# Performance work log

Hardware: AMD Instinct MI355X
Metric: run time of the kernel (lower is better)

## Reference

```python
import jax, jax.numpy as jnp
import numpy as np

B, T, C = 8, 1024, 768
NH = 12
HD = C // NH  # 64


def setup_inputs() -> dict:
    key = jax.random.key(0)
    k1, k2, k3 = jax.random.split(key, 3)
    x = jax.random.normal(k1, (B, T, C), dtype=jnp.float32)
    w_attn = jax.random.normal(k2, (C, 3 * C), dtype=jnp.float32) * 0.02
    b_attn = jnp.zeros((3 * C,), dtype=jnp.float32)
    w_proj = jax.random.normal(k3, (C, C), dtype=jnp.float32) * 0.02
    b_proj = jnp.zeros((C,), dtype=jnp.float32)
    return {"x": x, "w_attn": w_attn, "b_attn": b_attn, "w_proj": w_proj, "b_proj": b_proj}


def reference(x, w_attn, b_attn, w_proj, b_proj):
    Bb, Tt, Cc = x.shape
    qkv = x @ w_attn + b_attn  # [B,T,3C]
    q, k, v = jnp.split(qkv, [Cc, 2 * Cc], axis=-1)
    # [B, NH, T, HD]
    q = q.reshape(Bb, Tt, NH, HD).swapaxes(1, 2)
    k = k.reshape(Bb, Tt, NH, HD).swapaxes(1, 2)
    v = v.reshape(Bb, Tt, NH, HD).swapaxes(1, 2)
    scale = 1.0 / jnp.sqrt(jnp.asarray(HD, dtype=x.dtype))
    att = jnp.einsum("bhqd,bhkd->bhqk", q, k) * scale  # [B,NH,T,T]
    causal = jnp.tril(jnp.ones((Tt, Tt), dtype=bool))[None, None]
    att = jnp.where(causal, att, jnp.asarray(-jnp.inf, dtype=att.dtype))
    att = jax.nn.softmax(att, axis=-1)
    y = jnp.einsum("bhqk,bhkd->bhqd", att, v)  # [B,NH,T,HD]
    y = y.swapaxes(1, 2).reshape(Bb, Tt, Cc)
    return y @ w_proj + b_proj
```

## Files before the change

kernel.cpp:

```cpp
#include <hip/hip_runtime.h>
#include <cstdint>
#include <cstddef>

typedef __attribute__((ext_vector_type(8))) short short8;
typedef __attribute__((ext_vector_type(4))) float f32x4;
typedef __attribute__((ext_vector_type(4))) unsigned short u16x4;

#define ASYNC16(gp, lp) \
  __builtin_amdgcn_global_load_lds((const __attribute__((address_space(1))) unsigned int*)(gp), \
                                   (__attribute__((address_space(3))) unsigned int*)(lp), 16, 0, 0)

__device__ __forceinline__ unsigned short f2b(float f) {
  union { float f; unsigned int u; } c; c.f = f;
  unsigned int u = c.u;
  return (unsigned short)((u + 0x7fffu + ((u >> 16) & 1u)) >> 16);
}


__global__ void cvt_bf16(const float* __restrict__ X, unsigned short* __restrict__ Y, int n) {
  int i = (blockIdx.x * 256 + threadIdx.x) * 4;
  if (i < n) {
    const float* px = X + i;
    float a = px[0], b = px[1], c = px[2], d = px[3];
    u16x4 u;
    u[0] = f2b(a); u[1] = f2b(b); u[2] = f2b(c); u[3] = f2b(d);
    *(u16x4*)(Y + i) = u;
  }
}

__global__ void transpose_cvt(const float* __restrict__ W, unsigned short* __restrict__ WT,
                              int Kd, int Nd) {
  __shared__ unsigned short Ts[64][65];
  int n0 = blockIdx.x * 64, k0 = blockIdx.y * 64;
  int tid = threadIdx.x;
  for (int idx = tid; idx < 4096; idx += 256) {
    int lr = idx >> 6, lc = idx & 63;
    Ts[lr][lc] = f2b(W[(size_t)(k0 + lr) * Nd + n0 + lc]);
  }
  __syncthreads();
  for (int idx = tid; idx < 4096; idx += 256) {
    int nr = idx >> 6, kc = idx & 63;
    WT[(size_t)(n0 + nr) * Kd + k0 + kc] = Ts[kc][nr];
  }
}


__global__ __launch_bounds__(256, 2) void gemm_qkv(
    const unsigned short* __restrict__ A,
    const unsigned short* __restrict__ Bt,
    const float* __restrict__ bias,
    unsigned short* __restrict__ q,
    unsigned short* __restrict__ k,
    unsigned short* __restrict__ vT)
{
  __shared__ unsigned short As[128 * 32];
  __shared__ unsigned short Bs[128 * 32];
  const int tid = threadIdx.x;
  const int w = tid >> 6, lane = tid & 63;
  const int wm = w >> 1, wn = w & 1;
  const int lr = lane & 15, lq = lane >> 4;
  const int m0 = blockIdx.x * 128, n0 = blockIdx.y * 128;
  const f32x4 fzero = {0.f, 0.f, 0.f, 0.f};

  f32x4 acc[4][4];
  for (int i = 0; i < 4; ++i) for (int j = 0; j < 4; ++j) acc[i][j] = fzero;

  for (int kk0 = 0; kk0 < 768; kk0 += 32) {
    __syncthreads();
    for (int c = 0; c < 2; ++c) {
      int base = (c * 4 + w) * 1024;
      int e = (base >> 1) + lane * 8;
      int row = e >> 5, kc = e & 31;
      ASYNC16(A  + (size_t)(m0 + row) * 768 + kk0 + kc, (char*)As + base);
      ASYNC16(Bt + (size_t)(n0 + row) * 768 + kk0 + kc, (char*)Bs + base);
    }
    __builtin_amdgcn_s_waitcnt(0);
    __syncthreads();

    short8 a[4], b[4];
    for (int i = 0; i < 4; ++i)
      a[i] = *(const short8*)(As + (wm * 64 + i * 16 + lr) * 32 + lq * 8);
    for (int j = 0; j < 4; ++j)
      b[j] = *(const short8*)(Bs + (wn * 64 + j * 16 + lr) * 32 + lq * 8);
    for (int i = 0; i < 4; ++i)
      for (int j = 0; j < 4; ++j)
        acc[i][j] = __builtin_amdgcn_mfma_f32_16x16x32_bf16(a[i], b[j], acc[i][j], 0, 0, 0);
  }

  const int colbase = n0 + wn * 64;
  const int sec = colbase / 768;
  const float QSCALE = 0.18033688011112042f;
  for (int j = 0; j < 4; ++j) {
    int col = colbase + j * 16 + lr;
    int cc = col - sec * 768;
    int h = cc >> 6, d = cc & 63;
    float bv = bias[col];
    for (int i = 0; i < 4; ++i) {
      int row0 = m0 + wm * 64 + i * 16 + lq * 4;
      int bidx = row0 >> 10, t0 = row0 & 1023;
      int bh = bidx * 12 + h;
      if (sec == 0) {
        for (int r = 0; r < 4; ++r)
          q[((size_t)bh * 1024 + t0 + r) * 64 + d] = f2b((acc[i][j][r] + bv) * QSCALE);
      } else if (sec == 1) {
        for (int r = 0; r < 4; ++r)
          k[((size_t)bh * 1024 + t0 + r) * 64 + d] = f2b(acc[i][j][r] + bv);
      } else {
        u16x4 pv;
        pv[0] = f2b(acc[i][j][0] + bv);
        pv[1] = f2b(acc[i][j][1] + bv);
        pv[2] = f2b(acc[i][j][2] + bv);
        pv[3] = f2b(acc[i][j][3] + bv);
        *(u16x4*)(vT + ((size_t)bh * 64 + d) * 1024 + t0) = pv;
      }
    }
  }
}


__global__ __launch_bounds__(256, 2) void attn(
    const unsigned short* __restrict__ q,
    const unsigned short* __restrict__ kk,
    const unsigned short* __restrict__ vT,
    unsigned short* __restrict__ y)
{
  __shared__ unsigned short Qs[64 * 72];
  __shared__ unsigned short Ks[64 * 72];
  __shared__ unsigned short Vt[64 * 72];
  __shared__ unsigned short Ps[4 * 16 * 72];

  const int tid = threadIdx.x;
  const int w = tid >> 6, lane = tid & 63;
  const int lr = lane & 15, lq = lane >> 4;
  const int g = blockIdx.x;
  const int bh = g % 96;
  const int qp = g / 96;
  const int b = bh / 12, h = bh - b * 12;
  const f32x4 fzero = {0.f, 0.f, 0.f, 0.f};

  unsigned short* Pw = Ps + w * 16 * 72;
  const unsigned short* kbase = kk + (size_t)bh * 65536;
  const unsigned short* vbase = vT + (size_t)bh * 65536;

  const int c0 = tid, c1 = tid + 256;
  short8 kreg[2], vreg[2];

  for (int half = 0; half < 2; ++half) {
    const int qt = half ? (15 - qp) : qp;
    const int q0 = qt * 64;

    __syncthreads();
    {
      const unsigned short* qptr = q + ((size_t)bh * 1024 + q0) * 64;
      short8 q0r = *(const short8*)(qptr + (size_t)c0 * 8);
      short8 q1r = *(const short8*)(qptr + (size_t)c1 * 8);
      *(short8*)(Qs + (c0 >> 3) * 72 + (c0 & 7) * 8) = q0r;
      *(short8*)(Qs + (c1 >> 3) * 72 + (c1 & 7) * 8) = q1r;
    }
    kreg[0] = *(const short8*)(kbase + (size_t)c0 * 8);
    kreg[1] = *(const short8*)(kbase + (size_t)c1 * 8);
    vreg[0] = *(const short8*)(vbase + (size_t)(c0 >> 3) * 1024 + (c0 & 7) * 8);
    vreg[1] = *(const short8*)(vbase + (size_t)(c1 >> 3) * 1024 + (c1 & 7) * 8);

    f32x4 o[4];
    float l_s[4];
    for (int jd = 0; jd < 4; ++jd) o[jd] = fzero;
    for (int r = 0; r < 4; ++r) l_s[r] = 0.0f;

    for (int kt = 0; kt <= qt; ++kt) {
      __syncthreads();
      *(short8*)(Ks + (c0 >> 3) * 72 + (c0 & 7) * 8) = kreg[0];
      *(short8*)(Ks + (c1 >> 3) * 72 + (c1 & 7) * 8) = kreg[1];
      *(short8*)(Vt + (c0 >> 3) * 72 + (c0 & 7) * 8) = vreg[0];
      *(short8*)(Vt + (c1 >> 3) * 72 + (c1 & 7) * 8) = vreg[1];
      __syncthreads();
      if (kt < qt) {
        const unsigned short* kp = kbase + (size_t)(kt + 1) * 4096;
        const unsigned short* vp = vbase + (size_t)(kt + 1) * 64;
        kreg[0] = *(const short8*)(kp + (size_t)c0 * 8);
        kreg[1] = *(const short8*)(kp + (size_t)c1 * 8);
        vreg[0] = *(const short8*)(vp + (size_t)(c0 >> 3) * 1024 + (c0 & 7) * 8);
        vreg[1] = *(const short8*)(vp + (size_t)(c1 >> 3) * 1024 + (c1 & 7) * 8);
      }

      f32x4 s[4];
      for (int j = 0; j < 4; ++j) s[j] = fzero;
      for (int ks = 0; ks < 2; ++ks) {
        short8 aq = *(const short8*)(Qs + (w * 16 + lr) * 72 + ks * 32 + lq * 8);
        short8 bk[4];
        for (int j = 0; j < 4; ++j)
          bk[j] = *(const short8*)(Ks + (j * 16 + lr) * 72 + ks * 32 + lq * 8);
        for (int j = 0; j < 4; ++j)
          s[j] = __builtin_amdgcn_mfma_f32_16x16x32_bf16(aq, bk[j], s[j], 0, 0, 0);
      }
      if (kt == qt) {
        int rowt = w * 16 + lq * 4;
        for (int j = 0; j < 4; ++j) {
          int colt = j * 16 + lr;
          for (int r = 0; r < 4; ++r)
            if (colt > rowt + r) s[j][r] = -1e30f;
        }
      }
      for (int r = 0; r < 4; ++r) {
        int prow = (lq * 4 + r) * 72;
        float acc = 0.0f;
        for (int j = 0; j < 4; ++j) {
          float p = __builtin_amdgcn_exp2f(s[j][r]);
          acc += p;
          union { float f; unsigned int u; } cv; cv.f = p;
          Pw[prow + j * 16 + lr] = (unsigned short)((cv.u + 0x8000u) >> 16);
        }
        l_s[r] += acc;
      }
      for (int ks = 0; ks < 2; ++ks) {
        short8 ap = *(const short8*)(Pw + lr * 72 + ks * 32 + lq * 8);
        short8 bv[4];
        for (int jd = 0; jd < 4; ++jd)
          bv[jd] = *(const short8*)(Vt + (jd * 16 + lr) * 72 + ks * 32 + lq * 8);
        for (int jd = 0; jd < 4; ++jd)
          o[jd] = __builtin_amdgcn_mfma_f32_16x16x32_bf16(ap, bv[jd], o[jd], 0, 0, 0);
      }
    }

    for (int r = 0; r < 4; ++r) {
      float lv = l_s[r];
      for (int off = 1; off < 16; off <<= 1)
        lv += __shfl_xor(lv, off, 16);
      l_s[r] = 1.0f / lv;
    }
    int t = q0 + w * 16 + lq * 4;
    for (int jd = 0; jd < 4; ++jd) {
      int d = jd * 16 + lr;
      for (int r = 0; r < 4; ++r)
        y[((size_t)b * 1024 + t + r) * 768 + h * 64 + d] = f2b(o[jd][r] * l_s[r]);
    }
  }
}


__global__ __launch_bounds__(256, 2) void gemm_proj(
    const unsigned short* __restrict__ A,
    const unsigned short* __restrict__ Bt,
    const float* __restrict__ bias,
    float* __restrict__ out)
{
  __shared__ unsigned short As[128 * 32];
  __shared__ unsigned short Bs[128 * 32];
  const int tid = threadIdx.x;
  const int w = tid >> 6, lane = tid & 63;
  const int wm = w >> 1, wn = w & 1;
  const int lr = lane & 15, lq = lane >> 4;
  const int m0 = blockIdx.x * 128, n0 = blockIdx.y * 128;
  const f32x4 fzero = {0.f, 0.f, 0.f, 0.f};

  f32x4 acc[4][4];
  for (int i = 0; i < 4; ++i) for (int j = 0; j < 4; ++j) acc[i][j] = fzero;

  for (int kk0 = 0; kk0 < 768; kk0 += 32) {
    __syncthreads();
    for (int c = 0; c < 2; ++c) {
      int base = (c * 4 + w) * 1024;
      int e = (base >> 1) + lane * 8;
      int row = e >> 5, kc = e & 31;
      ASYNC16(A  + (size_t)(m0 + row) * 768 + kk0 + kc, (char*)As + base);
      ASYNC16(Bt + (size_t)(n0 + row) * 768 + kk0 + kc, (char*)Bs + base);
    }
    __builtin_amdgcn_s_waitcnt(0);
    __syncthreads();

    short8 a[4], b[4];
    for (int i = 0; i < 4; ++i)
      a[i] = *(const short8*)(As + (wm * 64 + i * 16 + lr) * 32 + lq * 8);
    for (int j = 0; j < 4; ++j)
      b[j] = *(const short8*)(Bs + (wn * 64 + j * 16 + lr) * 32 + lq * 8);
    for (int i = 0; i < 4; ++i)
      for (int j = 0; j < 4; ++j)
        acc[i][j] = __builtin_amdgcn_mfma_f32_16x16x32_bf16(a[i], b[j], acc[i][j], 0, 0, 0);
  }

  for (int j = 0; j < 4; ++j) {
    int col = n0 + wn * 64 + j * 16 + lr;
    float bv = bias[col];
    for (int i = 0; i < 4; ++i) {
      int row0 = m0 + wm * 64 + i * 16 + lq * 4;
      for (int r = 0; r < 4; ++r)
        out[(size_t)(row0 + r) * 768 + col] = acc[i][j][r] + bv;
    }
  }
}


extern "C" void kernel_launch(void* const* d_in, const int* in_sizes, int n_in,
                              void* d_out, int out_size, void* d_ws, size_t ws_size,
                              hipStream_t stream) {
  const float* x      = (const float*)d_in[0];
  const float* w_attn = (const float*)d_in[1];
  const float* b_attn = (const float*)d_in[2];
  const float* w_proj = (const float*)d_in[3];
  const float* b_proj = (const float*)d_in[4];
  float* out = (float*)d_out;

  char* p = (char*)d_ws;
  unsigned short* xb  = (unsigned short*)p; p += (size_t)8192 * 768 * 2;
  unsigned short* waT = (unsigned short*)p; p += (size_t)2304 * 768 * 2;
  unsigned short* wpT = (unsigned short*)p; p += (size_t)768 * 768 * 2;
  unsigned short* qb  = (unsigned short*)p; p += (size_t)96 * 1024 * 64 * 2;
  unsigned short* kb  = (unsigned short*)p; p += (size_t)96 * 1024 * 64 * 2;
  unsigned short* vTb = (unsigned short*)p; p += (size_t)96 * 64 * 1024 * 2;
  unsigned short* yb  = (unsigned short*)p; p += (size_t)8192 * 768 * 2;

  cvt_bf16<<<6144, 256, 0, stream>>>(x, xb, 8192 * 768);
  transpose_cvt<<<dim3(36, 12), 256, 0, stream>>>(w_attn, waT, 768, 2304);
  transpose_cvt<<<dim3(12, 12), 256, 0, stream>>>(w_proj, wpT, 768, 768);
  gemm_qkv<<<dim3(64, 18), 256, 0, stream>>>(xb, waT, b_attn, qb, kb, vTb);
  attn<<<768, 256, 0, stream>>>(qb, kb, vTb, yb);
  gemm_proj<<<dim3(64, 6), 256, 0, stream>>>(yb, wpT, b_proj, out);
}
```

Before: 196.1 us.

## Double-buffer LDS tiles in QKV and projection GEMMs with async prefetch

Both GEMM kernels now keep two LDS buffers per operand and issue the async global-to-LDS loads for the next K tile before computing on the current one. Explicit vmcnt waits and raw s_barrier replace the full waitcnt(0) plus syncthreads, so load latency can overlap the MFMA work. Launch bounds are raised to 4 blocks per CU, which limits registers and doubles LDS per block. The hand-written waitcnt and barrier ordering is fragile, and the tighter register budget may cause spills.

```diff
diff --git a/kernel.cpp b/kernel.cpp
--- a/kernel.cpp
+++ b/kernel.cpp
@@ -45,7 +45,7 @@
 }
 
 
-__global__ __launch_bounds__(256, 2) void gemm_qkv(
+__global__ __launch_bounds__(256, 4) void gemm_qkv(
     const unsigned short* __restrict__ A,
     const unsigned short* __restrict__ Bt,
     const float* __restrict__ bias,
@@ -53,8 +53,8 @@
     unsigned short* __restrict__ k,
     unsigned short* __restrict__ vT)
 {
-  __shared__ unsigned short As[128 * 32];
-  __shared__ unsigned short Bs[128 * 32];
+  __shared__ unsigned short As[2 * 4096];
+  __shared__ unsigned short Bs[2 * 4096];
   const int tid = threadIdx.x;
   const int w = tid >> 6, lane = tid & 63;
   const int wm = w >> 1, wn = w & 1;
@@ -65,23 +65,41 @@
   f32x4 acc[4][4];
   for (int i = 0; i < 4; ++i) for (int j = 0; j < 4; ++j) acc[i][j] = fzero;
 
-  for (int kk0 = 0; kk0 < 768; kk0 += 32) {
-    __syncthreads();
-    for (int c = 0; c < 2; ++c) {
-      int base = (c * 4 + w) * 1024;
-      int e = (base >> 1) + lane * 8;
-      int row = e >> 5, kc = e & 31;
-      ASYNC16(A  + (size_t)(m0 + row) * 768 + kk0 + kc, (char*)As + base);
-      ASYNC16(Bt + (size_t)(n0 + row) * 768 + kk0 + kc, (char*)Bs + base);
-    }
-    __builtin_amdgcn_s_waitcnt(0);
-    __syncthreads();
-
+  int sbase[2], srow[2], skc[2];
+  for (int c = 0; c < 2; ++c) {
+    sbase[c] = (c * 4 + w) * 1024;
+    int e = (sbase[c] >> 1) + lane * 8;
+    srow[c] = e >> 5; skc[c] = e & 31;
+  }
+
+  for (int c = 0; c < 2; ++c) {
+    ASYNC16(A  + (size_t)(m0 + srow[c]) * 768 + skc[c], (char*)As + sbase[c]);
+    ASYNC16(Bt + (size_t)(n0 + srow[c]) * 768 + skc[c], (char*)Bs + sbase[c]);
+  }
+
+  for (int kt = 0; kt < 24; ++kt) {
+    const int cur = kt & 1;
+    asm volatile("s_barrier" ::: "memory");
+    if (kt < 23) {
+      const int kk0 = (kt + 1) * 32;
+      const int dst = (cur ^ 1) * 8192;
+      for (int c = 0; c < 2; ++c) {
+        ASYNC16(A  + (size_t)(m0 + srow[c]) * 768 + kk0 + skc[c], (char*)As + dst + sbase[c]);
+        ASYNC16(Bt + (size_t)(n0 + srow[c]) * 768 + kk0 + skc[c], (char*)Bs + dst + sbase[c]);
+      }
+      asm volatile("s_waitcnt vmcnt(4)" ::: "memory");
+    } else {
+      asm volatile("s_waitcnt vmcnt(0)" ::: "memory");
+    }
+    asm volatile("s_barrier" ::: "memory");
+
+    const unsigned short* Ar = As + cur * 4096;
+    const unsigned short* Br = Bs + cur * 4096;
     short8 a[4], b[4];
     for (int i = 0; i < 4; ++i)
-      a[i] = *(const short8*)(As + (wm * 64 + i * 16 + lr) * 32 + lq * 8);
+      a[i] = *(const short8*)(Ar + (wm * 64 + i * 16 + lr) * 32 + lq * 8);
     for (int j = 0; j < 4; ++j)
-      b[j] = *(const short8*)(Bs + (wn * 64 + j * 16 + lr) * 32 + lq * 8);
+      b[j] = *(const short8*)(Br + (wn * 64 + j * 16 + lr) * 32 + lq * 8);
     for (int i = 0; i < 4; ++i)
       for (int j = 0; j < 4; ++j)
         acc[i][j] = __builtin_amdgcn_mfma_f32_16x16x32_bf16(a[i], b[j], acc[i][j], 0, 0, 0);
@@ -238,14 +256,14 @@
 }
 
 
-__global__ __launch_bounds__(256, 2) void gemm_proj(
+__global__ __launch_bounds__(256, 4) void gemm_proj(
     const unsigned short* __restrict__ A,
     const unsigned short* __restrict__ Bt,
     const float* __restrict__ bias,
     float* __restrict__ out)
 {
-  __shared__ unsigned short As[128 * 32];
-  __shared__ unsigned short Bs[128 * 32];
+  __shared__ unsigned short As[2 * 4096];
+  __shared__ unsigned short Bs[2 * 4096];
   const int tid = threadIdx.x;
   const int w = tid >> 6, lane = tid & 63;
   const int wm = w >> 1, wn = w & 1;
@@ -256,23 +274,41 @@
   f32x4 acc[4][4];
   for (int i = 0; i < 4; ++i) for (int j = 0; j < 4; ++j) acc[i][j] = fzero;
 
-  for (int kk0 = 0; kk0 < 768; kk0 += 32) {
-    __syncthreads();
-    for (int c = 0; c < 2; ++c) {
-      int base = (c * 4 + w) * 1024;
-      int e = (base >> 1) + lane * 8;
-      int row = e >> 5, kc = e & 31;
-      ASYNC16(A  + (size_t)(m0 + row) * 768 + kk0 + kc, (char*)As + base);
-      ASYNC16(Bt + (size_t)(n0 + row) * 768 + kk0 + kc, (char*)Bs + base);
-    }
-    __builtin_amdgcn_s_waitcnt(0);
-    __syncthreads();
-
+  int sbase[2], srow[2], skc[2];
+  for (int c = 0; c < 2; ++c) {
+    sbase[c] = (c * 4 + w) * 1024;
+    int e = (sbase[c] >> 1) + lane * 8;
+    srow[c] = e >> 5; skc[c] = e & 31;
+  }
+
+  for (int c = 0; c < 2; ++c) {
+    ASYNC16(A  + (size_t)(m0 + srow[c]) * 768 + skc[c], (char*)As + sbase[c]);
+    ASYNC16(Bt + (size_t)(n0 + srow[c]) * 768 + skc[c], (char*)Bs + sbase[c]);
+  }
+
+  for (int kt = 0; kt < 24; ++kt) {
+    const int cur = kt & 1;
+    asm volatile("s_barrier" ::: "memory");
+    if (kt < 23) {
+      const int kk0 = (kt + 1) * 32;
+      const int dst = (cur ^ 1) * 8192;
+      for (int c = 0; c < 2; ++c) {
+        ASYNC16(A  + (size_t)(m0 + srow[c]) * 768 + kk0 + skc[c], (char*)As + dst + sbase[c]);
+        ASYNC16(Bt + (size_t)(n0 + srow[c]) * 768 + kk0 + skc[c], (char*)Bs + dst + sbase[c]);
+      }
+      asm volatile("s_waitcnt vmcnt(4)" ::: "memory");
+    } else {
+      asm volatile("s_waitcnt vmcnt(0)" ::: "memory");
+    }
+    asm volatile("s_barrier" ::: "memory");
+
+    const unsigned short* Ar = As + cur * 4096;
+    const unsigned short* Br = Bs + cur * 4096;
     short8 a[4], b[4];
     for (int i = 0; i < 4; ++i)
-      a[i] = *(const short8*)(As + (wm * 64 + i * 16 + lr) * 32 + lq * 8);
+      a[i] = *(const short8*)(Ar + (wm * 64 + i * 16 + lr) * 32 + lq * 8);
     for (int j = 0; j < 4; ++j)
-      b[j] = *(const short8*)(Bs + (wn * 64 + j * 16 + lr) * 32 + lq * 8);
+      b[j] = *(const short8*)(Br + (wn * 64 + j * 16 + lr) * 32 + lq * 8);
     for (int i = 0; i < 4; ++i)
       for (int j = 0; j < 4; ++j)
         acc[i][j] = __builtin_amdgcn_mfma_f32_16x16x32_bf16(a[i], b[j], acc[i][j], 0, 0, 0);
```

After: 194.6 us. No clear change (-0.8%).

## Register-prefetch GEMM tiles into padded LDS instead of synchronous async loads

Applied to the files above, without the earlier changes.

Both GEMM kernels stop using global_load_lds followed by a full waitcnt. Each thread now prefetches the next K-slice of A and B into registers while the MFMAs for the current slice run, then writes that slice to LDS. The LDS row stride is padded from 32 to 40 elements to reduce bank conflicts on fragment reads, and the occupancy hint goes from 2 to 3 blocks per CU. The aim is to hide global-memory latency behind compute, at the cost of extra VGPRs and an explicit register-to-LDS store step.

```diff
diff --git a/kernel.cpp b/kernel.cpp
--- a/kernel.cpp
+++ b/kernel.cpp
@@ -5,10 +5,6 @@
 typedef __attribute__((ext_vector_type(8))) short short8;
 typedef __attribute__((ext_vector_type(4))) float f32x4;
 typedef __attribute__((ext_vector_type(4))) unsigned short u16x4;
-
-#define ASYNC16(gp, lp) \
-  __builtin_amdgcn_global_load_lds((const __attribute__((address_space(1))) unsigned int*)(gp), \
-                                   (__attribute__((address_space(3))) unsigned int*)(lp), 16, 0, 0)
 
 __device__ __forceinline__ unsigned short f2b(float f) {
   union { float f; unsigned int u; } c; c.f = f;
@@ -45,7 +41,7 @@
 }
 
 
-__global__ __launch_bounds__(256, 2) void gemm_qkv(
+__global__ __launch_bounds__(256, 3) void gemm_qkv(
     const unsigned short* __restrict__ A,
     const unsigned short* __restrict__ Bt,
     const float* __restrict__ bias,
@@ -53,8 +49,8 @@
     unsigned short* __restrict__ k,
     unsigned short* __restrict__ vT)
 {
-  __shared__ unsigned short As[128 * 32];
-  __shared__ unsigned short Bs[128 * 32];
+  __shared__ unsigned short As[128 * 40];
+  __shared__ unsigned short Bs[128 * 40];
   const int tid = threadIdx.x;
   const int w = tid >> 6, lane = tid & 63;
   const int wm = w >> 1, wn = w & 1;
@@ -65,23 +61,37 @@
   f32x4 acc[4][4];
   for (int i = 0; i < 4; ++i) for (int j = 0; j < 4; ++j) acc[i][j] = fzero;
 
-  for (int kk0 = 0; kk0 < 768; kk0 += 32) {
-    __syncthreads();
-    for (int c = 0; c < 2; ++c) {
-      int base = (c * 4 + w) * 1024;
-      int e = (base >> 1) + lane * 8;
-      int row = e >> 5, kc = e & 31;
-      ASYNC16(A  + (size_t)(m0 + row) * 768 + kk0 + kc, (char*)As + base);
-      ASYNC16(Bt + (size_t)(n0 + row) * 768 + kk0 + kc, (char*)Bs + base);
-    }
-    __builtin_amdgcn_s_waitcnt(0);
-    __syncthreads();
-
+  const int srow = tid >> 2;
+  const int skc  = (tid & 3) * 8;
+  const unsigned short* Ap0 = A  + (size_t)(m0 + srow) * 768 + skc;
+  const unsigned short* Ap1 = A  + (size_t)(m0 + srow + 64) * 768 + skc;
+  const unsigned short* Bp0 = Bt + (size_t)(n0 + srow) * 768 + skc;
+  const unsigned short* Bp1 = Bt + (size_t)(n0 + srow + 64) * 768 + skc;
+
+  short8 ra0 = *(const short8*)(Ap0);
+  short8 ra1 = *(const short8*)(Ap1);
+  short8 rb0 = *(const short8*)(Bp0);
+  short8 rb1 = *(const short8*)(Bp1);
+
+  for (int kt = 0; kt < 24; ++kt) {
+    __syncthreads();
+    *(short8*)(As + srow * 40 + skc)        = ra0;
+    *(short8*)(As + (srow + 64) * 40 + skc) = ra1;
+    *(short8*)(Bs + srow * 40 + skc)        = rb0;
+    *(short8*)(Bs + (srow + 64) * 40 + skc) = rb1;
+    __syncthreads();
+    if (kt < 23) {
+      const int kk0 = (kt + 1) * 32;
+      ra0 = *(const short8*)(Ap0 + kk0);
+      ra1 = *(const short8*)(Ap1 + kk0);
+      rb0 = *(const short8*)(Bp0 + kk0);
+      rb1 = *(const short8*)(Bp1 + kk0);
+    }
     short8 a[4], b[4];
     for (int i = 0; i < 4; ++i)
-      a[i] = *(const short8*)(As + (wm * 64 + i * 16 + lr) * 32 + lq * 8);
+      a[i] = *(const short8*)(As + (wm * 64 + i * 16 + lr) * 40 + lq * 8);
     for (int j = 0; j < 4; ++j)
-      b[j] = *(const short8*)(Bs + (wn * 64 + j * 16 + lr) * 32 + lq * 8);
+      b[j] = *(const short8*)(Bs + (wn * 64 + j * 16 + lr) * 40 + lq * 8);
     for (int i = 0; i < 4; ++i)
       for (int j = 0; j < 4; ++j)
         acc[i][j] = __builtin_amdgcn_mfma_f32_16x16x32_bf16(a[i], b[j], acc[i][j], 0, 0, 0);
@@ -238,14 +248,14 @@
 }
 
 
-__global__ __launch_bounds__(256, 2) void gemm_proj(
+__global__ __launch_bounds__(256, 3) void gemm_proj(
     const unsigned short* __restrict__ A,
     const unsigned short* __restrict__ Bt,
     const float* __restrict__ bias,
     float* __restrict__ out)
 {
-  __shared__ unsigned short As[128 * 32];
-  __shared__ unsigned short Bs[128 * 32];
+  __shared__ unsigned short As[128 * 40];
+  __shared__ unsigned short Bs[128 * 40];
   const int tid = threadIdx.x;
   const int w = tid >> 6, lane = tid & 63;
   const int wm = w >> 1, wn = w & 1;
@@ -256,23 +266,37 @@
   f32x4 acc[4][4];
   for (int i = 0; i < 4; ++i) for (int j = 0; j < 4; ++j) acc[i][j] = fzero;
 
-  for (int kk0 = 0; kk0 < 768; kk0 += 32) {
-    __syncthreads();
-    for (int c = 0; c < 2; ++c) {
-      int base = (c * 4 + w) * 1024;
-      int e = (base >> 1) + lane * 8;
-      int row = e >> 5, kc = e & 31;
-      ASYNC16(A  + (size_t)(m0 + row) * 768 + kk0 + kc, (char*)As + base);
-      ASYNC16(Bt + (size_t)(n0 + row) * 768 + kk0 + kc, (char*)Bs + base);
-    }
-    __builtin_amdgcn_s_waitcnt(0);
-    __syncthreads();
-
+  const int srow = tid >> 2;
+  const int skc  = (tid & 3) * 8;
+  const unsigned short* Ap0 = A  + (size_t)(m0 + srow) * 768 + skc;
+  const unsigned short* Ap1 = A  + (size_t)(m0 + srow + 64) * 768 + skc;
+  const unsigned short* Bp0 = Bt + (size_t)(n0 + srow) * 768 + skc;
+  const unsigned short* Bp1 = Bt + (size_t)(n0 + srow + 64) * 768 + skc;
+
+  short8 ra0 = *(const short8*)(Ap0);
+  short8 ra1 = *(const short8*)(Ap1);
+  short8 rb0 = *(const short8*)(Bp0);
+  short8 rb1 = *(const short8*)(Bp1);
+
+  for (int kt = 0; kt < 24; ++kt) {
+    __syncthreads();
+    *(short8*)(As + srow * 40 + skc)        = ra0;
+    *(short8*)(As + (srow + 64) * 40 + skc) = ra1;
+    *(short8*)(Bs + srow * 40 + skc)        = rb0;
+    *(short8*)(Bs + (srow + 64) * 40 + skc) = rb1;
+    __syncthreads();
+    if (kt < 23) {
+      const int kk0 = (kt + 1) * 32;
+      ra0 = *(const short8*)(Ap0 + kk0);
+      ra1 = *(const short8*)(Ap1 + kk0);
+      rb0 = *(const short8*)(Bp0 + kk0);
+      rb1 = *(const short8*)(Bp1 + kk0);
+    }
     short8 a[4], b[4];
     for (int i = 0; i < 4; ++i)
-      a[i] = *(const short8*)(As + (wm * 64 + i * 16 + lr) * 32 + lq * 8);
+      a[i] = *(const short8*)(As + (wm * 64 + i * 16 + lr) * 40 + lq * 8);
     for (int j = 0; j < 4; ++j)
-      b[j] = *(const short8*)(Bs + (wn * 64 + j * 16 + lr) * 32 + lq * 8);
+      b[j] = *(const short8*)(Bs + (wn * 64 + j * 16 + lr) * 40 + lq * 8);
     for (int i = 0; i < 4; ++i)
       for (int j = 0; j < 4; ++j)
         acc[i][j] = __builtin_amdgcn_mfma_f32_16x16x32_bf16(a[i], b[j], acc[i][j], 0, 0, 0);
```

After: 194.9 us. No clear change (-0.6%).
